# Kernel tuning notes

Measured on AMD Instinct MI355X. Metric: run time of the kernel, lower is better.

Reference implementation:

```python
import jax, jax.numpy as jnp
import numpy as np

L, N, E, H = 1024, 8, 512, 8  # tgt/src len, batch, embed_dim, num_heads


def setup_inputs() -> dict:
    key = jax.random.key(0)
    ks = jax.random.split(key, 5)
    query = jax.random.normal(ks[0], (L, N, E), dtype=jnp.float32)
    # binary same-agent mask over (tgt, src) positions
    agent_aware_mask = (jax.random.uniform(ks[1], (L, L)) > 0.5).astype(jnp.float32)
    bound = 1.0 / np.sqrt(E)
    # agent-aware dot_product self-attn packs q,k,v,q_same,k_same -> (5E, E)
    in_proj_weight = jax.random.uniform(ks[2], (5 * E, E), jnp.float32, -bound, bound)
    in_proj_bias = jnp.zeros((5 * E,), jnp.float32)
    out_proj_weight = jax.random.uniform(ks[3], (E, E), jnp.float32, -bound, bound)
    out_proj_bias = jnp.zeros((E,), jnp.float32)
    return dict(query=query, in_proj_weight=in_proj_weight, in_proj_bias=in_proj_bias,
                out_proj_weight=out_proj_weight, out_proj_bias=out_proj_bias,
                agent_aware_mask=agent_aware_mask)


def _to_heads(x, tgt_len, bsz, num_heads, head_dim):
    # (L, N, E) -> (N*H, L, head_dim), matching torch's view+transpose
    return x.reshape(tgt_len, bsz * num_heads, head_dim).transpose(1, 0, 2)


def reference(query, in_proj_weight, in_proj_bias, out_proj_weight, out_proj_bias, agent_aware_mask):
    tgt_len, bsz, embed_dim = query.shape
    num_heads = H
    head_dim = embed_dim // num_heads
    scaling = float(head_dim) ** -0.5
    temperature = 1.0

    # packed input projection, chunked into 5: q, k, v, q_same, k_same
    proj = query @ in_proj_weight.T + in_proj_bias
    q, k, v, q_same, k_same = jnp.split(proj, 5, axis=-1)
    q = q * scaling
    q_same = q_same * scaling

    qh = _to_heads(q, tgt_len, bsz, num_heads, head_dim)
    kh = _to_heads(k, tgt_len, bsz, num_heads, head_dim)
    vh = _to_heads(v, tgt_len, bsz, num_heads, head_dim)
    qsh = _to_heads(q_same, tgt_len, bsz, num_heads, head_dim)
    ksh = _to_heads(k_same, tgt_len, bsz, num_heads, head_dim)

    attn_diff = jnp.einsum('bld,bsd->bls', qh, kh)    # cross-agent scores
    attn_same = jnp.einsum('bld,bsd->bls', qsh, ksh)  # same-agent scores

    mask = agent_aware_mask[None, :, :]  # broadcast over (N*H)
    logits = (attn_diff * (1.0 - mask) + attn_same * mask) / temperature

    attn_weights = jax.nn.softmax(logits, axis=-1)
    out = jnp.einsum('bls,bsd->bld', attn_weights, vh)  # (N*H, L, hd)
    out = out.transpose(1, 0, 2).reshape(tgt_len, bsz, embed_dim)
    return out @ out_proj_weight.T + out_proj_bias
```

## Files before the change

kernel.cpp:

```cpp
#include <hip/hip_runtime.h>


typedef float f32x4 __attribute__((ext_vector_type(4)));
typedef short s16x8 __attribute__((ext_vector_type(8)));
typedef unsigned short u16;
typedef u16 u16x4 __attribute__((ext_vector_type(4)));
typedef unsigned int u32x2 __attribute__((ext_vector_type(2)));

#define MFMA16(a, b, c) __builtin_amdgcn_mfma_f32_16x16x32_bf16((a), (b), (c), 0, 0, 0)

__device__ __forceinline__ u16 f2bf(float f) {
  __bf16 h = (__bf16)f;
  return __builtin_bit_cast(u16, h);
}
__device__ __forceinline__ unsigned int pack2(float a, float b) {
  return (unsigned int)f2bf(a) | ((unsigned int)f2bf(b) << 16);
}
__device__ __forceinline__ void gload_lds16(const u16* g, u16* l) {
  __builtin_amdgcn_global_load_lds(
      (const __attribute__((address_space(1))) void*)g,
      (__attribute__((address_space(3))) void*)l, 16, 0, 0);
}

__global__ __launch_bounds__(256) void cvt_swz(const float* __restrict__ in,
                                               u16* __restrict__ out, int n4) {
  int i = blockIdx.x * 256 + threadIdx.x;
  if (i >= n4) return;
  f32x4 v = *(const f32x4*)(in + (size_t)i * 4);
  int e = i << 2;
  int r = e >> 9;
  int k = e & 511;
  int ks = k ^ (((r >> 1) & 3) << 3);
  u16x4 o;
  o[0] = f2bf(v[0]); o[1] = f2bf(v[1]); o[2] = f2bf(v[2]); o[3] = f2bf(v[3]);
  *(u16x4*)(out + ((size_t)r << 9) + ks) = o;
}

__global__ __launch_bounds__(256) void mask_pack(const float* __restrict__ m,
                                                 unsigned long long* __restrict__ out) {
  int i = blockIdx.x * 256 + threadIdx.x;
  unsigned long long b = __ballot(m[i] != 0.0f);
  if ((threadIdx.x & 63) == 0) out[i >> 6] = b;
}

__global__ __launch_bounds__(256) void gemm_inproj(
    const u16* __restrict__ X, const u16* __restrict__ W,
    const float* __restrict__ bias,
    u16* __restrict__ Qg, u16* __restrict__ Kg, u16* __restrict__ Vtg,
    u16* __restrict__ Qsg, u16* __restrict__ Ksg) {
  __shared__ __attribute__((aligned(16))) u16 At[128 * 64];
  __shared__ __attribute__((aligned(16))) u16 Bt[128 * 64];
  const int tid = threadIdx.x;
  const int lane = tid & 63, w = tid >> 6;
  const int lr = lane & 15, lq = lane >> 4;
  const int wr = w >> 1, wc = w & 1;
  const int tm = blockIdx.x * 128, tn = blockIdx.y * 128;

  f32x4 acc[4][4] = {};

  for (int k0 = 0; k0 < 512; k0 += 64) {
    if (k0) __syncthreads();
#pragma unroll
    for (int j = 0; j < 4; ++j) {
      const int c = (w * 4 + j) * 64 + lane;
      const int row = c >> 3;
      const int col = (c & 7) * 8;
      gload_lds16(X + (size_t)(tm + row) * 512 + k0 + col, At + (w * 4 + j) * 512);
      gload_lds16(W + (size_t)(tn + row) * 512 + k0 + col, Bt + (w * 4 + j) * 512);
    }
    __syncthreads();
#pragma unroll
    for (int ks = 0; ks < 2; ++ks) {
      s16x8 af[4], bf[4];
#pragma unroll
      for (int mi = 0; mi < 4; ++mi) {
        const int row = wr * 64 + mi * 16 + lr;
        const int col = ks * 32 + ((lq * 8) ^ ((((tm + row) >> 1) & 3) << 3));
        af[mi] = *(const s16x8*)(At + row * 64 + col);
      }
#pragma unroll
      for (int ni = 0; ni < 4; ++ni) {
        const int row = wc * 64 + ni * 16 + lr;
        const int col = ks * 32 + ((lq * 8) ^ ((((tn + row) >> 1) & 3) << 3));
        bf[ni] = *(const s16x8*)(Bt + row * 64 + col);
      }
#pragma unroll
      for (int mi = 0; mi < 4; ++mi)
#pragma unroll
        for (int ni = 0; ni < 4; ++ni)
          acc[mi][ni] = MFMA16(af[mi], bf[ni], acc[mi][ni]);
    }
  }

  const int chunk = tn >> 9;
  const float qscale = 0.125f * 1.4426950408889634f;
#pragma unroll
  for (int ni = 0; ni < 4; ++ni) {
    const int gc = tn + wc * 64 + ni * 16 + lr;
    const float bv = bias[gc];
    const int e = gc & 511;
    const int hh = e >> 6, dd = e & 63;
#pragma unroll
    for (int mi = 0; mi < 4; ++mi) {
#pragma unroll
      for (int r = 0; r < 4; ++r) {
        const int gr = tm + wr * 64 + mi * 16 + lq * 4 + r;
        const int l = gr >> 3, nn = gr & 7;
        const size_t base = (size_t)(nn * 8 + hh) << 16;
        float v = acc[mi][ni][r] + bv;
        if (chunk == 0) {
          Qg[base + l * 64 + dd] = f2bf(v * qscale);
        } else if (chunk == 3) {
          Qsg[base + l * 64 + dd] = f2bf(v * qscale);
        } else if (chunk == 1) {
          Kg[base + l * 64 + (dd ^ ((l & 7) << 3))] = f2bf(v);
        } else if (chunk == 4) {
          Ksg[base + l * 64 + (dd ^ ((l & 7) << 3))] = f2bf(v);
        } else {
          Vtg[base + (size_t)dd * 1024 + (l ^ ((dd & 7) << 3))] = f2bf(v);
        }
      }
    }
  }
}

__global__ __launch_bounds__(256, 4) void attn_kernel(
    const u16* __restrict__ Qg, const u16* __restrict__ Kg,
    const u16* __restrict__ Vtg, const u16* __restrict__ Qsg,
    const u16* __restrict__ Ksg, const unsigned long long* __restrict__ Mp,
    u16* __restrict__ Og) {
  __shared__ __attribute__((aligned(16))) u16 Kt[64 * 64];
  __shared__ __attribute__((aligned(16))) u16 Kst[64 * 64];
  __shared__ __attribute__((aligned(16))) u16 Vt[64 * 64];
  __shared__ __attribute__((aligned(16))) u16 Pl[4][16 * 72];

  const int tid = threadIdx.x;
  const int lane = tid & 63, w = tid >> 6;
  const int lr = lane & 15, lq = lane >> 4;
  const int bh = blockIdx.y;
  const int q0 = blockIdx.x * 64;
  const size_t bbase = (size_t)bh << 16;
  const int nn = bh >> 3, hh = bh & 7;
  const int l = q0 + w * 16 + lr;

  s16x8 qf[2], qsf[2];
#pragma unroll
  for (int ks = 0; ks < 2; ++ks) {
    qf[ks] = *(const s16x8*)(Qg + bbase + (size_t)l * 64 + ks * 32 + lq * 8);
    qsf[ks] = *(const s16x8*)(Qsg + bbase + (size_t)l * 64 + ks * 32 + lq * 8);
  }

  f32x4 oacc[4] = {};
  float m_run = -1e30f, l_run = 0.f;

  for (int t = 0; t < 16; ++t) {
    const int s0 = t * 64;
    if (t) __syncthreads();
#pragma unroll
    for (int j = 0; j < 2; ++j) {
      const int cb = (w * 2 + j) * 64;
      const int c = cb + lane;
      const int row = c >> 3, col = (c & 7) * 8;
      gload_lds16(Kg + bbase + (size_t)(s0 + row) * 64 + col, Kt + cb * 8);
      gload_lds16(Ksg + bbase + (size_t)(s0 + row) * 64 + col, Kst + cb * 8);
      gload_lds16(Vtg + bbase + (size_t)row * 1024 + s0 + col, Vt + cb * 8);
    }
    const unsigned long long mw = Mp[(size_t)l * 16 + t];
    __syncthreads();

    f32x4 sd[4] = {}, ss[4] = {};
    __builtin_amdgcn_s_setprio(1);
#pragma unroll
    for (int smi = 0; smi < 4; ++smi) {
      const int srow = smi * 16 + lr;
      const int sw = (srow & 7) << 3;
#pragma unroll
      for (int ks = 0; ks < 2; ++ks) {
        const int off = srow * 64 + ((ks * 32 + lq * 8) ^ sw);
        const s16x8 kf = *(const s16x8*)(Kt + off);
        const s16x8 kfs = *(const s16x8*)(Kst + off);
        sd[smi] = MFMA16(kf, qf[ks], sd[smi]);
        ss[smi] = MFMA16(kfs, qsf[ks], ss[smi]);
      }
    }
    __builtin_amdgcn_s_setprio(0);

    float mt = -1e30f;
#pragma unroll
    for (int smi = 0; smi < 4; ++smi) {
      const unsigned nib = (unsigned)(mw >> (smi * 16 + lq * 4));
#pragma unroll
      for (int r = 0; r < 4; ++r) {
        const float v = (nib & (1u << r)) ? ss[smi][r] : sd[smi][r];
        sd[smi][r] = v;
        mt = fmaxf(mt, v);
      }
    }
    mt = fmaxf(mt, __shfl_xor(mt, 16));
    mt = fmaxf(mt, __shfl_xor(mt, 32));

    if (!__all(mt <= m_run + 8.0f)) {
      const float mnew = fmaxf(m_run, mt);
      const float sc = exp2f(m_run - mnew);
      m_run = mnew;
      l_run *= sc;
#pragma unroll
      for (int dmi = 0; dmi < 4; ++dmi) oacc[dmi] *= sc;
    }

    float ts = 0.f;
#pragma unroll
    for (int smi = 0; smi < 4; ++smi)
#pragma unroll
      for (int r = 0; r < 4; ++r) {
        const float p = exp2f(sd[smi][r] - m_run);
        sd[smi][r] = p;
        ts += p;
      }
#pragma unroll
    for (int smi = 0; smi < 4; ++smi) {
      u32x2 pw;
      pw[0] = pack2(sd[smi][0], sd[smi][1]);
      pw[1] = pack2(sd[smi][2], sd[smi][3]);
      *(u32x2*)(&Pl[w][lr * 72 + smi * 16 + lq * 4]) = pw;
    }
    ts += __shfl_xor(ts, 16);
    ts += __shfl_xor(ts, 32);
    l_run += ts;

    asm volatile("s_waitcnt lgkmcnt(0)" ::: "memory");
    __builtin_amdgcn_sched_barrier(0);

    __builtin_amdgcn_s_setprio(1);
#pragma unroll
    for (int ks = 0; ks < 2; ++ks) {
      const s16x8 pf = *(const s16x8*)(&Pl[w][lr * 72 + ks * 32 + lq * 8]);
#pragma unroll
      for (int dmi = 0; dmi < 4; ++dmi) {
        const int d = dmi * 16 + lr;
        const s16x8 vf =
            *(const s16x8*)(Vt + d * 64 + ((ks * 32 + lq * 8) ^ ((d & 7) << 3)));
        oacc[dmi] = MFMA16(vf, pf, oacc[dmi]);
      }
    }
    __builtin_amdgcn_s_setprio(0);
  }

  const float inv = 1.0f / l_run;
  const int rout = l * 8 + nn;
  const int swzr = ((rout >> 1) & 3) << 3;
#pragma unroll
  for (int dmi = 0; dmi < 4; ++dmi) {
    u16x4 o;
#pragma unroll
    for (int r = 0; r < 4; ++r) o[r] = f2bf(oacc[dmi][r] * inv);
    const int kout = (hh * 64 + dmi * 16 + lq * 4) ^ swzr;
    *(u16x4*)(Og + (size_t)rout * 512 + kout) = o;
  }
}

__global__ __launch_bounds__(256) void gemm_outproj(
    const u16* __restrict__ A, const u16* __restrict__ W,
    const float* __restrict__ bias, float* __restrict__ out) {
  __shared__ __attribute__((aligned(16))) u16 At[128 * 64];
  __shared__ __attribute__((aligned(16))) u16 Bt[64 * 64];
  const int tid = threadIdx.x;
  const int lane = tid & 63, w = tid >> 6;
  const int lr = lane & 15, lq = lane >> 4;
  const int wr = w >> 1, wc = w & 1;
  const int tm = blockIdx.x * 128, tn = blockIdx.y * 64;

  f32x4 acc[4][2] = {};

  for (int k0 = 0; k0 < 512; k0 += 64) {
    if (k0) __syncthreads();
#pragma unroll
    for (int j = 0; j < 4; ++j) {
      const int c = (w * 4 + j) * 64 + lane;
      const int row = c >> 3;
      const int col = (c & 7) * 8;
      gload_lds16(A + (size_t)(tm + row) * 512 + k0 + col, At + (w * 4 + j) * 512);
    }
#pragma unroll
    for (int j = 0; j < 2; ++j) {
      const int c = (w * 2 + j) * 64 + lane;
      const int row = c >> 3;
      const int col = (c & 7) * 8;
      gload_lds16(W + (size_t)(tn + row) * 512 + k0 + col, Bt + (w * 2 + j) * 512);
    }
    __syncthreads();
#pragma unroll
    for (int ks = 0; ks < 2; ++ks) {
      s16x8 af[4], bf[2];
#pragma unroll
      for (int mi = 0; mi < 4; ++mi) {
        const int row = wr * 64 + mi * 16 + lr;
        const int col = ks * 32 + ((lq * 8) ^ ((((tm + row) >> 1) & 3) << 3));
        af[mi] = *(const s16x8*)(At + row * 64 + col);
      }
#pragma unroll
      for (int ni = 0; ni < 2; ++ni) {
        const int row = wc * 32 + ni * 16 + lr;
        const int col = ks * 32 + ((lq * 8) ^ ((((tn + row) >> 1) & 3) << 3));
        bf[ni] = *(const s16x8*)(Bt + row * 64 + col);
      }
#pragma unroll
      for (int mi = 0; mi < 4; ++mi)
#pragma unroll
        for (int ni = 0; ni < 2; ++ni)
          acc[mi][ni] = MFMA16(af[mi], bf[ni], acc[mi][ni]);
    }
  }

#pragma unroll
  for (int ni = 0; ni < 2; ++ni) {
    const int gc = tn + wc * 32 + ni * 16 + lr;
    const float bv = bias[gc];
#pragma unroll
    for (int mi = 0; mi < 4; ++mi)
#pragma unroll
      for (int r = 0; r < 4; ++r) {
        const int gr = tm + wr * 64 + mi * 16 + lq * 4 + r;
        out[(size_t)gr * 512 + gc] = acc[mi][ni][r] + bv;
      }
  }
}

extern "C" void kernel_launch(void* const* d_in, const int* in_sizes, int n_in,
                              void* d_out, int out_size, void* d_ws, size_t ws_size,
                              hipStream_t stream) {
  const float* query = (const float*)d_in[0];
  const float* w_in = (const float*)d_in[1];
  const float* b_in = (const float*)d_in[2];
  const float* w_out = (const float*)d_in[3];
  const float* b_out = (const float*)d_in[4];
  const float* mask = (const float*)d_in[5];

  char* ws = (char*)d_ws;
  u16* Xbf = (u16*)(ws + 0);
  u16* Wbf = (u16*)(ws + 8388608);
  u16* Wobf = (u16*)(ws + 11010048);
  u16* Qg = (u16*)(ws + 11534336);
  u16* Kg = (u16*)(ws + 19922944);
  u16* Vtg = (u16*)(ws + 28311552);
  u16* Qsg = (u16*)(ws + 36700160);
  u16* Ksg = (u16*)(ws + 45088768);
  u16* Og = (u16*)(ws + 53477376);
  unsigned long long* Mp = (unsigned long long*)(ws + 0);

  hipLaunchKernelGGL(cvt_swz, dim3(4096), dim3(256), 0, stream, query, Xbf, 1048576);
  hipLaunchKernelGGL(cvt_swz, dim3(1280), dim3(256), 0, stream, w_in, Wbf, 327680);
  hipLaunchKernelGGL(cvt_swz, dim3(256), dim3(256), 0, stream, w_out, Wobf, 65536);
  hipLaunchKernelGGL(gemm_inproj, dim3(64, 20), dim3(256), 0, stream,
                     Xbf, Wbf, b_in, Qg, Kg, Vtg, Qsg, Ksg);
  hipLaunchKernelGGL(mask_pack, dim3(4096), dim3(256), 0, stream, mask, Mp);
  hipLaunchKernelGGL(attn_kernel, dim3(16, 64), dim3(256), 0, stream,
                     Qg, Kg, Vtg, Qsg, Ksg, Mp, Og);
  hipLaunchKernelGGL(gemm_outproj, dim3(64, 8), dim3(256), 0, stream,
                     Og, Wobf, b_out, (float*)d_out);
}
```

Measured before the change: 200.7 us.

## Process two query row-tiles per wave in attention to reuse K/V tiles

```diff
diff --git a/kernel.cpp b/kernel.cpp
--- a/kernel.cpp
+++ b/kernel.cpp
@@ -5,16 +5,12 @@
 typedef short s16x8 __attribute__((ext_vector_type(8)));
 typedef unsigned short u16;
 typedef u16 u16x4 __attribute__((ext_vector_type(4)));
-typedef unsigned int u32x2 __attribute__((ext_vector_type(2)));
 
 #define MFMA16(a, b, c) __builtin_amdgcn_mfma_f32_16x16x32_bf16((a), (b), (c), 0, 0, 0)
 
 __device__ __forceinline__ u16 f2bf(float f) {
   __bf16 h = (__bf16)f;
   return __builtin_bit_cast(u16, h);
-}
-__device__ __forceinline__ unsigned int pack2(float a, float b) {
-  return (unsigned int)f2bf(a) | ((unsigned int)f2bf(b) << 16);
 }
 __device__ __forceinline__ void gload_lds16(const u16* g, u16* l) {
   __builtin_amdgcn_global_load_lds(
@@ -124,7 +120,7 @@
   }
 }
 
-__global__ __launch_bounds__(256, 4) void attn_kernel(
+__global__ __launch_bounds__(256) void attn_kernel(
     const u16* __restrict__ Qg, const u16* __restrict__ Kg,
     const u16* __restrict__ Vtg, const u16* __restrict__ Qsg,
     const u16* __restrict__ Ksg, const unsigned long long* __restrict__ Mp,
@@ -132,26 +128,32 @@
   __shared__ __attribute__((aligned(16))) u16 Kt[64 * 64];
   __shared__ __attribute__((aligned(16))) u16 Kst[64 * 64];
   __shared__ __attribute__((aligned(16))) u16 Vt[64 * 64];
-  __shared__ __attribute__((aligned(16))) u16 Pl[4][16 * 72];
+  __shared__ __attribute__((aligned(16))) u16 Pl[4][32 * 72];
 
   const int tid = threadIdx.x;
   const int lane = tid & 63, w = tid >> 6;
   const int lr = lane & 15, lq = lane >> 4;
-  const int bh = blockIdx.y;
-  const int q0 = blockIdx.x * 64;
+  const int id = blockIdx.x;
+  const int g = id >> 3;
+  const int bh = (id & 7) * 8 + (g & 7);
+  const int q0 = (g >> 3) * 128;
   const size_t bbase = (size_t)bh << 16;
   const int nn = bh >> 3, hh = bh & 7;
-  const int l = q0 + w * 16 + lr;
-
-  s16x8 qf[2], qsf[2];
-#pragma unroll
-  for (int ks = 0; ks < 2; ++ks) {
-    qf[ks] = *(const s16x8*)(Qg + bbase + (size_t)l * 64 + ks * 32 + lq * 8);
-    qsf[ks] = *(const s16x8*)(Qsg + bbase + (size_t)l * 64 + ks * 32 + lq * 8);
-  }
-
-  f32x4 oacc[4] = {};
-  float m_run = -1e30f, l_run = 0.f;
+
+  s16x8 qf[2][2], qsf[2][2];
+#pragma unroll
+  for (int nl = 0; nl < 2; ++nl) {
+    const int l = q0 + w * 32 + nl * 16 + lr;
+#pragma unroll
+    for (int ks = 0; ks < 2; ++ks) {
+      qf[nl][ks] = *(const s16x8*)(Qg + bbase + (size_t)l * 64 + ks * 32 + lq * 8);
+      qsf[nl][ks] = *(const s16x8*)(Qsg + bbase + (size_t)l * 64 + ks * 32 + lq * 8);
+    }
+  }
+
+  f32x4 oacc[4][2] = {};
+  float m_run[2] = {-1e30f, -1e30f};
+  float l_run[2] = {0.f, 0.f};
 
   for (int t = 0; t < 16; ++t) {
     const int s0 = t * 64;
@@ -165,10 +167,16 @@
       gload_lds16(Ksg + bbase + (size_t)(s0 + row) * 64 + col, Kst + cb * 8);
       gload_lds16(Vtg + bbase + (size_t)row * 1024 + s0 + col, Vt + cb * 8);
     }
-    const unsigned long long mw = Mp[(size_t)l * 16 + t];
+    const int lm0 = q0 + w * 32 + lr;
+    const unsigned long long mw0 = Mp[(size_t)lm0 * 16 + t];
+    const unsigned long long mw1 = Mp[(size_t)(lm0 + 16) * 16 + t];
     __syncthreads();
 
-    f32x4 sd[4] = {}, ss[4] = {};
+    f32x4 sd[4][2], ss[4][2];
+#pragma unroll
+    for (int smi = 0; smi < 4; ++smi)
+#pragma unroll
+      for (int nl = 0; nl < 2; ++nl) { sd[smi][nl] = (f32x4)0.f; ss[smi][nl] = (f32x4)0.f; }
     __builtin_amdgcn_s_setprio(1);
 #pragma unroll
     for (int smi = 0; smi < 4; ++smi) {
@@ -179,54 +187,74 @@
         const int off = srow * 64 + ((ks * 32 + lq * 8) ^ sw);
         const s16x8 kf = *(const s16x8*)(Kt + off);
         const s16x8 kfs = *(const s16x8*)(Kst + off);
-        sd[smi] = MFMA16(kf, qf[ks], sd[smi]);
-        ss[smi] = MFMA16(kfs, qsf[ks], ss[smi]);
+#pragma unroll
+        for (int nl = 0; nl < 2; ++nl) {
+          sd[smi][nl] = MFMA16(kf, qf[nl][ks], sd[smi][nl]);
+          ss[smi][nl] = MFMA16(kfs, qsf[nl][ks], ss[smi][nl]);
+        }
       }
     }
     __builtin_amdgcn_s_setprio(0);
 
-    float mt = -1e30f;
+    float mt[2] = {-1e30f, -1e30f};
 #pragma unroll
     for (int smi = 0; smi < 4; ++smi) {
-      const unsigned nib = (unsigned)(mw >> (smi * 16 + lq * 4));
-#pragma unroll
-      for (int r = 0; r < 4; ++r) {
-        const float v = (nib & (1u << r)) ? ss[smi][r] : sd[smi][r];
-        sd[smi][r] = v;
-        mt = fmaxf(mt, v);
-      }
-    }
-    mt = fmaxf(mt, __shfl_xor(mt, 16));
-    mt = fmaxf(mt, __shfl_xor(mt, 32));
-
-    if (!__all(mt <= m_run + 8.0f)) {
-      const float mnew = fmaxf(m_run, mt);
-      const float sc = exp2f(m_run - mnew);
-      m_run = mnew;
-      l_run *= sc;
-#pragma unroll
-      for (int dmi = 0; dmi < 4; ++dmi) oacc[dmi] *= sc;
-    }
-
-    float ts = 0.f;
+#pragma unroll
+      for (int nl = 0; nl < 2; ++nl) {
+        const unsigned nib =
+            (unsigned)((nl ? mw1 : mw0) >> (smi * 16 + lq * 4)) & 15u;
+#pragma unroll
+        for (int r = 0; r < 4; ++r) {
+          const float v = (nib & (1u << r)) ? ss[smi][nl][r] : sd[smi][nl][r];
+          sd[smi][nl][r] = v;
+          mt[nl] = fmaxf(mt[nl], v);
+        }
+      }
+    }
+#pragma unroll
+    for (int nl = 0; nl < 2; ++nl) {
+      float m2 = fmaxf(mt[nl], __shfl_xor(mt[nl], 16));
+      m2 = fmaxf(m2, __shfl_xor(m2, 32));
+      mt[nl] = m2;
+    }
+#pragma unroll
+    for (int nl = 0; nl < 2; ++nl) {
+      if (!__all(mt[nl] <= m_run[nl] + 8.0f)) {
+        const float mnew = fmaxf(m_run[nl], mt[nl]);
+        const float sc = exp2f(m_run[nl] - mnew);
+        m_run[nl] = mnew;
+        l_run[nl] *= sc;
+#pragma unroll
+        for (int dmi = 0; dmi < 4; ++dmi) oacc[dmi][nl] *= sc;
+      }
+    }
+
+    float ts[2] = {0.f, 0.f};
 #pragma unroll
     for (int smi = 0; smi < 4; ++smi)
 #pragma unroll
-      for (int r = 0; r < 4; ++r) {
-        const float p = exp2f(sd[smi][r] - m_run);
-        sd[smi][r] = p;
-        ts += p;
-      }
-#pragma unroll
-    for (int smi = 0; smi < 4; ++smi) {
-      u32x2 pw;
-      pw[0] = pack2(sd[smi][0], sd[smi][1]);
-      pw[1] = pack2(sd[smi][2], sd[smi][3]);
-      *(u32x2*)(&Pl[w][lr * 72 + smi * 16 + lq * 4]) = pw;
-    }
-    ts += __shfl_xor(ts, 16);
-    ts += __shfl_xor(ts, 32);
-    l_run += ts;
+      for (int nl = 0; nl < 2; ++nl)
+#pragma unroll
+        for (int r = 0; r < 4; ++r) {
+          const float p = exp2f(sd[smi][nl][r] - m_run[nl]);
+          sd[smi][nl][r] = p;
+          ts[nl] += p;
+        }
+#pragma unroll
+    for (int smi = 0; smi < 4; ++smi)
+#pragma unroll
+      for (int nl = 0; nl < 2; ++nl) {
+        u16x4 pw;
+#pragma unroll
+        for (int r = 0; r < 4; ++r) pw[r] = f2bf(sd[smi][nl][r]);
+        *(u16x4*)(&Pl[w][(nl * 16 + lr) * 72 + smi * 16 + lq * 4]) = pw;
+      }
+#pragma unroll
+    for (int nl = 0; nl < 2; ++nl) {
+      float s2 = ts[nl] + __shfl_xor(ts[nl], 16);
+      s2 += __shfl_xor(s2, 32);
+      l_run[nl] += s2;
+    }
 
     asm volatile("s_waitcnt lgkmcnt(0)" ::: "memory");
     __builtin_amdgcn_sched_barrier(0);
@@ -234,28 +262,37 @@
     __builtin_amdgcn_s_setprio(1);
 #pragma unroll
     for (int ks = 0; ks < 2; ++ks) {
-      const s16x8 pf = *(const s16x8*)(&Pl[w][lr * 72 + ks * 32 + lq * 8]);
+      s16x8 pf[2];
+#pragma unroll
+      for (int nl = 0; nl < 2; ++nl)
+        pf[nl] = *(const s16x8*)(&Pl[w][(nl * 16 + lr) * 72 + ks * 32 + lq * 8]);
 #pragma unroll
       for (int dmi = 0; dmi < 4; ++dmi) {
         const int d = dmi * 16 + lr;
         const s16x8 vf =
             *(const s16x8*)(Vt + d * 64 + ((ks * 32 + lq * 8) ^ ((d & 7) << 3)));
-        oacc[dmi] = MFMA16(vf, pf, oacc[dmi]);
+#pragma unroll
+        for (int nl = 0; nl < 2; ++nl)
+          oacc[dmi][nl] = MFMA16(vf, pf[nl], oacc[dmi][nl]);
       }
     }
     __builtin_amdgcn_s_setprio(0);
   }
 
-  const float inv = 1.0f / l_run;
-  const int rout = l * 8 + nn;
-  const int swzr = ((rout >> 1) & 3) << 3;
-#pragma unroll
-  for (int dmi = 0; dmi < 4; ++dmi) {
-    u16x4 o;
-#pragma unroll
-    for (int r = 0; r < 4; ++r) o[r] = f2bf(oacc[dmi][r] * inv);
-    const int kout = (hh * 64 + dmi * 16 + lq * 4) ^ swzr;
-    *(u16x4*)(Og + (size_t)rout * 512 + kout) = o;
+#pragma unroll
+  for (int nl = 0; nl < 2; ++nl) {
+    const float inv = 1.0f / l_run[nl];
+    const int l = q0 + w * 32 + nl * 16 + lr;
+    const int rout = l * 8 + nn;
+    const int swzr = ((rout >> 1) & 3) << 3;
+#pragma unroll
+    for (int dmi = 0; dmi < 4; ++dmi) {
+      u16x4 o;
+#pragma unroll
+      for (int r = 0; r < 4; ++r) o[r] = f2bf(oacc[dmi][nl][r] * inv);
+      const int kout = (hh * 64 + dmi * 16 + lq * 4) ^ swzr;
+      *(u16x4*)(Og + (size_t)rout * 512 + kout) = o;
+    }
   }
 }
 
@@ -354,7 +391,7 @@
   hipLaunchKernelGGL(gemm_inproj, dim3(64, 20), dim3(256), 0, stream,
                      Xbf, Wbf, b_in, Qg, Kg, Vtg, Qsg, Ksg);
   hipLaunchKernelGGL(mask_pack, dim3(4096), dim3(256), 0, stream, mask, Mp);
-  hipLaunchKernelGGL(attn_kernel, dim3(16, 64), dim3(256), 0, stream,
+  hipLaunchKernelGGL(attn_kernel, dim3(512), dim3(256), 0, stream,
                      Qg, Kg, Vtg, Qsg, Ksg, Mp, Og);
   hipLaunchKernelGGL(gemm_outproj, dim3(64, 8), dim3(256), 0, stream,
                      Og, Wobf, b_out, (float*)d_out);
```

Result: no change. 201.0 us (+0.2%).
